# Performance work log

Measured on AMD Instinct MI355X. Metric: run time of the kernel, lower is better.

Reference implementation:

```python
import jax, jax.numpy as jnp
import numpy as np


def _hann_filter(P):
    # ramp filter built in spatial domain (Kak & Slaney) times fftshifted Hann window
    n = np.concatenate([np.arange(1, P // 2 + 1, 2), np.arange(P // 2 - 1, 0, -2)]).astype(np.float64)
    f = np.zeros(P, np.float64)
    f[0] = 0.25
    f[1::2] = -1.0 / (np.pi * n) ** 2
    ramp = 2.0 * np.real(np.fft.fft(f))
    filt = ramp * np.fft.fftshift(np.hanning(P))
    return jnp.asarray(filt, jnp.float32)


def _fbp(sino, angles, circle):
    B, A, L = sino.shape
    P = max(64, int(2 ** np.ceil(np.log2(2 * L))))  # img_size_padded
    center = L // 2
    # --- FFT filtering (filtered=True) ---
    filt = _hann_filter(P)
    sino_p = jnp.pad(sino, ((0, 0), (0, 0), (0, P - L)))
    sino_f = jnp.real(jnp.fft.ifft(jnp.fft.fft(sino_p, axis=-1) * filt, axis=-1))[:, :, :L]
    # --- back-projection: emulate grid_sample(bilinear, align_corners=True, padding zeros) ---
    x, y = jnp.meshgrid(jnp.arange(L, dtype=jnp.float32) - center,
                        jnp.arange(L, dtype=jnp.float32) - center, indexing='ij')
    th = angles + jnp.pi / 2
    t = x[None] * jnp.cos(th)[:, None, None] + y[None] * jnp.sin(th)[:, None, None]  # [A,L,L]
    # t_norm = 2t/(L-1); align_corners pixel coord = (t_norm+1)/2*(L-1) = t + (L-1)/2
    u = t + (L - 1) / 2.0
    i0 = jnp.floor(u)
    frac = u - i0
    i0i = i0.astype(jnp.int32)
    i1i = i0i + 1
    v0 = (i0i >= 0) & (i0i < L)
    v1 = (i1i >= 0) & (i1i < L)
    w0 = jnp.where(v0, 1.0 - frac, 0.0)  # zero-padding: kill OOB taps
    w1 = jnp.where(v1, frac, 0.0)
    aidx = jnp.arange(A)[:, None, None]
    g0 = sino_f[:, aidx, jnp.clip(i0i, 0, L - 1)]  # [B,A,L,L]
    g1 = sino_f[:, aidx, jnp.clip(i1i, 0, L - 1)]
    recon = jnp.sum(w0[None] * g0 + w1[None] * g1, axis=1)  # [B,L,L]
    if circle:
        Y, X = np.ogrid[:L, :L]
        mask = jnp.asarray(np.sqrt((X - center) ** 2 + (Y - center) ** 2) > center)
        recon = jnp.where(mask[None], 0.0, recon)
    return recon


def setup_inputs() -> dict:
    key = jax.random.key(0)
    sino = jax.random.normal(key, (2, 181, 512), dtype=jnp.float32)
    angles = jnp.linspace(0.0, np.pi, 181).astype(jnp.float32)
    return {"sino": sino, "angles": angles, "circle": 1}


def reference(sino, angles, circle):
    return _fbp(sino, angles, circle)
```

## Files before the change

kernel.cpp:

```cpp
#include <hip/hip_runtime.h>
#include <math.h>

#define OFF_FILT 0
#define OFF_HR   1024
#define OFF_CTH  2048
#define OFF_STH  2304
#define OFF_SF   4096

__device__ __forceinline__ float cos2pi(float x) {
  return __builtin_amdgcn_cosf(x);
}

__global__ __launch_bounds__(256) void k_filt(const float* __restrict__ angles,
                                              float* __restrict__ ws,
                                              float* __restrict__ out) {
  const int t = threadIdx.x & 63;
  const int k = blockIdx.x * 4 + (threadIdx.x >> 6);
  float acc = 0.f;
#pragma unroll
  for (int q = 0; q < 8; q++) {
    int tt = t + 64 * q;
    int n = (tt < 256) ? (2 * tt + 1) : (1023 - 2 * tt);
    float pin = 3.14159265358979f * (float)n;
    float cf = -1.0f / (pin * pin);
    int r = ((2 * tt + 1) * k) & 1023;
    acc = fmaf(cf, cos2pi((float)r * (1.0f / 1024.0f)), acc);
  }
#pragma unroll
  for (int o = 32; o; o >>= 1) acc += __shfl_down(acc, o, 64);
  if (t == 0) {
    float ramp = 0.5f + 2.0f * acc;
    int ks = (k + 512) & 1023;
    float hann = 0.5f - 0.5f * cos2pi((float)ks * (1.0f / 1023.0f));
    ws[OFF_FILT + k] = ramp * hann;
  }
  if (blockIdx.x == 0 && threadIdx.x < 181) {
    float th = angles[threadIdx.x] + 1.5707963267948966f;
    ws[OFF_CTH + threadIdx.x] = cosf(th);
    ws[OFF_STH + threadIdx.x] = sinf(th);
  }
  const float4 z4 = make_float4(0.f, 0.f, 0.f, 0.f);
  float4* o4 = (float4*)out;
  int idx = blockIdx.x * 256 + threadIdx.x;
  o4[idx] = z4;
  o4[idx + 65536] = z4;
}

__global__ __launch_bounds__(256) void k_hr(float* __restrict__ ws) {
  const int t = threadIdx.x & 63;
  const int m = blockIdx.x * 4 + (threadIdx.x >> 6);
  float acc = 0.f;
  int r = (t * m) & 1023;
  const int step = (64 * m) & 1023;
#pragma unroll
  for (int q = 0; q < 16; q++) {
    acc = fmaf(ws[OFF_FILT + t + 64 * q],
               cos2pi((float)r * (1.0f / 1024.0f)), acc);
    r = (r + step) & 1023;
  }
#pragma unroll
  for (int o = 32; o; o >>= 1) acc += __shfl_down(acc, o, 64);
  if (t == 0) ws[OFF_HR + m] = acc * (1.0f / 1024.0f);
}

__global__ __launch_bounds__(64) void k_conv(const float* __restrict__ sino,
                                             float* __restrict__ ws) {
  __shared__ float s_s0[512];
  __shared__ float s_s1[512];
  __shared__ float s_hr[1024];
  const int t = threadIdx.x;
  const int a = blockIdx.x;
  const float4* r0 = (const float4*)(sino + (size_t)a * 512);
  const float4* r1 = (const float4*)(sino + (size_t)(181 + a) * 512);
  ((float4*)s_s0)[t] = r0[t];
  ((float4*)s_s0)[t + 64] = r0[t + 64];
  ((float4*)s_s1)[t] = r1[t];
  ((float4*)s_s1)[t + 64] = r1[t + 64];
  const float4* hr4 = (const float4*)(ws + OFF_HR);
#pragma unroll
  for (int q = 0; q < 4; q++) ((float4*)s_hr)[t + 64 * q] = hr4[t + 64 * q];
  __syncthreads();

  const int base = blockIdx.y * 256 + t * 4;
  float acc0[4] = {0.f, 0.f, 0.f, 0.f};
  float acc1[4] = {0.f, 0.f, 0.f, 0.f};
  const float4* SH = (const float4*)s_hr;
  const float4* S0 = (const float4*)s_s0;
  const float4* S1 = (const float4*)s_s1;
  for (int j8 = 0; j8 < 512; j8 += 8) {
    float4 sa0 = S0[j8 >> 2];
    float4 sb0 = S0[(j8 >> 2) + 1];
    float4 sa1 = S1[j8 >> 2];
    float4 sb1 = S1[(j8 >> 2) + 1];
    int w = base - j8;
    float4 h0 = SH[((w - 8) & 1023) >> 2];
    float4 h1 = SH[((w - 4) & 1023) >> 2];
    float4 h2 = SH[(w & 1023) >> 2];
    float qq[12] = {h0.x, h0.y, h0.z, h0.w, h1.x, h1.y,
                    h1.z, h1.w, h2.x, h2.y, h2.z, h2.w};
    float v0[8] = {sa0.x, sa0.y, sa0.z, sa0.w, sb0.x, sb0.y, sb0.z, sb0.w};
    float v1[8] = {sa1.x, sa1.y, sa1.z, sa1.w, sb1.x, sb1.y, sb1.z, sb1.w};
#pragma unroll
    for (int jj = 0; jj < 8; jj++) {
#pragma unroll
      for (int m = 0; m < 4; m++) {
        acc0[m] = fmaf(v0[jj], qq[8 + m - jj], acc0[m]);
        acc1[m] = fmaf(v1[jj], qq[8 + m - jj], acc1[m]);
      }
    }
  }
  float* dst = ws + OFF_SF + (size_t)a * 1024 + base * 2;
  ((float4*)dst)[0] = make_float4(acc0[0], acc1[0], acc0[1], acc1[1]);
  ((float4*)dst)[1] = make_float4(acc0[2], acc1[2], acc0[3], acc1[3]);
}

#define PAD   108
#define ROWE  728
#define CHUNK 4
__global__ __launch_bounds__(512) void k_bp(const float* __restrict__ ws,
                                            const int* __restrict__ circ,
                                            float* __restrict__ out) {
  __shared__ float2 srow[CHUNK * ROWE];
  const int j = threadIdx.x;
  const int i = blockIdx.x;
  const int abase = blockIdx.y * 91;
  const int acnt = min(91, 181 - abase);
  const float xc = (float)(i - 256);
  const float yc = (float)(j - 256);
  const float* __restrict__ cth = ws + OFF_CTH;
  const float* __restrict__ sth = ws + OFF_STH;
  float acc0 = 0.f, acc1 = 0.f;

  const float2 z2 = make_float2(0.f, 0.f);
#pragma unroll
  for (int r = 0; r < CHUNK; r++) {
    if (j < PAD) srow[r * ROWE + j] = z2;
    if (j < ROWE - PAD - 512) srow[r * ROWE + PAD + 512 + j] = z2;
  }

  const int r0 = j >> 8, r1 = r0 + 2;
  const int p0 = (j & 255) * 2;
  const int col = j & 255;
  const float4* __restrict__ G = (const float4*)(ws + OFF_SF);
  float4* SW0 = (float4*)&srow[r0 * ROWE + PAD + p0];
  float4* SW1 = (float4*)&srow[r1 * ROWE + PAD + p0];
  const int rowcap = abase + acnt - 1;

  int A = abase;
  float4 pre0 = G[min(A + r0, rowcap) * 256 + col];
  float4 pre1 = G[min(A + r1, rowcap) * 256 + col];

  for (int c = 0; c < 23; c++) {
    __syncthreads();
    *SW0 = pre0;
    *SW1 = pre1;
    const int An = A + CHUNK;
    if (c < 22) {
      pre0 = G[min(An + r0, rowcap) * 256 + col];
      pre1 = G[min(An + r1, rowcap) * 256 + col];
    }
    __syncthreads();
    const int nv = min(CHUNK, abase + acnt - A);
#pragma unroll
    for (int r = 0; r < CHUNK; r++) {
      if (r >= nv) break;
      const int a = A + r;
      const float c_ = cth[a];
      const float s_ = sth[a];
      float u = fmaf(xc, c_, fmaf(yc, s_, 255.5f + (float)PAD));
      float fl = floorf(u);
      float fr = u - fl;
      int b = (int)fl;
      const float2* rp = &srow[r * ROWE];
      float2 t0 = rp[b];
      float2 t1 = rp[b + 1];
      float w0 = 1.0f - fr;
      acc0 = fmaf(w0, t0.x, fmaf(fr, t1.x, acc0));
      acc1 = fmaf(w0, t0.y, fmaf(fr, t1.y, acc1));
    }
    A = An;
  }
  const int dx = j - 256, dy = i - 256;
  const bool msk = (circ[0] != 0) && (dx * dx + dy * dy > 65536);
  if (!msk) {
    const size_t o = (size_t)i * 512 + j;
    atomicAdd(&out[o], acc0);
    atomicAdd(&out[262144 + o], acc1);
  }
}

extern "C" void kernel_launch(void* const* d_in, const int* in_sizes, int n_in,
                              void* d_out, int out_size, void* d_ws, size_t ws_size,
                              hipStream_t stream) {
  const float* sino = (const float*)d_in[0];
  const float* angles = (const float*)d_in[1];
  const int* circ = (const int*)d_in[2];
  float* ws = (float*)d_ws;
  float* out = (float*)d_out;

  hipLaunchKernelGGL(k_filt, dim3(256),    dim3(256), 0, stream, angles, ws, out);
  hipLaunchKernelGGL(k_hr,   dim3(256),    dim3(256), 0, stream, ws);
  hipLaunchKernelGGL(k_conv, dim3(181, 2), dim3(64),  0, stream, sino, ws);
  hipLaunchKernelGGL(k_bp,   dim3(512, 2), dim3(512), 0, stream, ws, circ, out);
}
```

Baseline: 95.04 us.

## Back-project two image rows per thread with larger angle chunks

Each back-projection block now computes two adjacent image rows (i0 and i0+1), so every staged sinogram chunk in shared memory serves twice as many pixels. The second row's coordinate is derived from the first by adding cos(theta). The angle chunk grows from 4 to 12 rows, which cuts the number of barrier pairs and lets six float4 prefetches per thread be in flight at once. The grid is halved to match. The cost is more registers and more shared memory per block (12 rows of 728 float2), which may lower occupancy, plus fewer blocks in total.

```diff
diff --git a/kernel.cpp b/kernel.cpp
--- a/kernel.cpp
+++ b/kernel.cpp
@@ -116,20 +116,20 @@
 
 #define PAD   108
 #define ROWE  728
-#define CHUNK 4
-__global__ __launch_bounds__(512) void k_bp(const float* __restrict__ ws,
-                                            const int* __restrict__ circ,
-                                            float* __restrict__ out) {
+#define CHUNK 12
+__global__ __launch_bounds__(512, 4) void k_bp(const float* __restrict__ ws,
+                                               const int* __restrict__ circ,
+                                               float* __restrict__ out) {
   __shared__ float2 srow[CHUNK * ROWE];
   const int j = threadIdx.x;
-  const int i = blockIdx.x;
+  const int i0 = blockIdx.x * 2;
   const int abase = blockIdx.y * 91;
   const int acnt = min(91, 181 - abase);
-  const float xc = (float)(i - 256);
+  const float xc = (float)(i0 - 256);
   const float yc = (float)(j - 256);
   const float* __restrict__ cth = ws + OFF_CTH;
   const float* __restrict__ sth = ws + OFF_STH;
-  float acc0 = 0.f, acc1 = 0.f;
+  float a00 = 0.f, a01 = 0.f, a10 = 0.f, a11 = 0.f;
 
   const float2 z2 = make_float2(0.f, 0.f);
 #pragma unroll
@@ -138,26 +138,27 @@
     if (j < ROWE - PAD - 512) srow[r * ROWE + PAD + 512 + j] = z2;
   }
 
-  const int r0 = j >> 8, r1 = r0 + 2;
-  const int p0 = (j & 255) * 2;
+  const int rb = j >> 8;
   const int col = j & 255;
   const float4* __restrict__ G = (const float4*)(ws + OFF_SF);
-  float4* SW0 = (float4*)&srow[r0 * ROWE + PAD + p0];
-  float4* SW1 = (float4*)&srow[r1 * ROWE + PAD + p0];
   const int rowcap = abase + acnt - 1;
 
   int A = abase;
-  float4 pre0 = G[min(A + r0, rowcap) * 256 + col];
-  float4 pre1 = G[min(A + r1, rowcap) * 256 + col];
-
-  for (int c = 0; c < 23; c++) {
+  float4 pre[6];
+#pragma unroll
+  for (int q = 0; q < 6; q++)
+    pre[q] = G[min(A + rb + 2 * q, rowcap) * 256 + col];
+
+  for (int c = 0; c < 8; c++) {
     __syncthreads();
-    *SW0 = pre0;
-    *SW1 = pre1;
+#pragma unroll
+    for (int q = 0; q < 6; q++)
+      *(float4*)&srow[(rb + 2 * q) * ROWE + PAD + 2 * col] = pre[q];
     const int An = A + CHUNK;
-    if (c < 22) {
-      pre0 = G[min(An + r0, rowcap) * 256 + col];
-      pre1 = G[min(An + r1, rowcap) * 256 + col];
+    if (c < 7) {
+#pragma unroll
+      for (int q = 0; q < 6; q++)
+        pre[q] = G[min(An + rb + 2 * q, rowcap) * 256 + col];
     }
     __syncthreads();
     const int nv = min(CHUNK, abase + acnt - A);
@@ -167,25 +168,36 @@
       const int a = A + r;
       const float c_ = cth[a];
       const float s_ = sth[a];
-      float u = fmaf(xc, c_, fmaf(yc, s_, 255.5f + (float)PAD));
-      float fl = floorf(u);
-      float fr = u - fl;
-      int b = (int)fl;
+      float u0 = fmaf(xc, c_, fmaf(yc, s_, 255.5f + (float)PAD));
+      float u1 = u0 + c_;
+      float fl0 = floorf(u0), fl1 = floorf(u1);
+      float fr0 = u0 - fl0, fr1 = u1 - fl1;
+      int b0 = (int)fl0, b1 = (int)fl1;
       const float2* rp = &srow[r * ROWE];
-      float2 t0 = rp[b];
-      float2 t1 = rp[b + 1];
-      float w0 = 1.0f - fr;
-      acc0 = fmaf(w0, t0.x, fmaf(fr, t1.x, acc0));
-      acc1 = fmaf(w0, t0.y, fmaf(fr, t1.y, acc1));
+      float2 p00 = rp[b0];
+      float2 p01 = rp[b0 + 1];
+      float2 p10 = rp[b1];
+      float2 p11 = rp[b1 + 1];
+      float w0 = 1.0f - fr0, w1 = 1.0f - fr1;
+      a00 = fmaf(w0, p00.x, fmaf(fr0, p01.x, a00));
+      a01 = fmaf(w0, p00.y, fmaf(fr0, p01.y, a01));
+      a10 = fmaf(w1, p10.x, fmaf(fr1, p11.x, a10));
+      a11 = fmaf(w1, p10.y, fmaf(fr1, p11.y, a11));
     }
     A = An;
   }
-  const int dx = j - 256, dy = i - 256;
-  const bool msk = (circ[0] != 0) && (dx * dx + dy * dy > 65536);
-  if (!msk) {
-    const size_t o = (size_t)i * 512 + j;
-    atomicAdd(&out[o], acc0);
-    atomicAdd(&out[262144 + o], acc1);
+
+  const int dx = j - 256;
+  const bool con = (circ[0] != 0);
+  const int dy0 = i0 - 256, dy1 = i0 + 1 - 256;
+  const size_t o0 = (size_t)i0 * 512 + j;
+  if (!(con && dx * dx + dy0 * dy0 > 65536)) {
+    atomicAdd(&out[o0], a00);
+    atomicAdd(&out[262144 + o0], a01);
+  }
+  if (!(con && dx * dx + dy1 * dy1 > 65536)) {
+    atomicAdd(&out[o0 + 512], a10);
+    atomicAdd(&out[262144 + o0 + 512], a11);
   }
 }
 
@@ -201,5 +213,5 @@
   hipLaunchKernelGGL(k_filt, dim3(256),    dim3(256), 0, stream, angles, ws, out);
   hipLaunchKernelGGL(k_hr,   dim3(256),    dim3(256), 0, stream, ws);
   hipLaunchKernelGGL(k_conv, dim3(181, 2), dim3(64),  0, stream, sino, ws);
-  hipLaunchKernelGGL(k_bp,   dim3(512, 2), dim3(512), 0, stream, ws, circ, out);
-}
+  hipLaunchKernelGGL(k_bp,   dim3(256, 2), dim3(512), 0, stream, ws, circ, out);
+}
```

Result: slower. 132.6 us (+39.6%).
